# Performance work log

Hardware: AMD Instinct MI355X
Metric: run time of the kernel (lower is better)

The kernel has to match this reference:

```python
import jax, jax.numpy as jnp
import numpy as np

B, L, D, V, M = 8, 64, 256, 4096, 16


def _norm(a):
    # torch .std(-1) uses ddof=1 (unbiased)
    return a / (1e-5 + jnp.std(a, axis=-1, keepdims=True, ddof=1))


def setup_inputs() -> dict:
    key = jax.random.key(0)
    ks = jax.random.split(key, 13)
    s = 0.05
    return {
        "x": jax.random.randint(ks[0], (B, L), 0, V),
        "z": jax.random.randint(ks[1], (B, L), 0, V),
        "embed_w": jax.random.normal(ks[2], (V, D), dtype=jnp.float32) * s,
        "init_w": jax.random.normal(ks[3], (D, M), dtype=jnp.float32) * s,
        "trans_w": jax.random.normal(ks[4], (D, D), dtype=jnp.float32) * s,
        "trans_b": jax.random.normal(ks[5], (D,), dtype=jnp.float32) * s,
        "core_w": jax.random.normal(ks[6], (D, D), dtype=jnp.float32) * s,
        "upd_w": jax.random.normal(ks[7], (D, D), dtype=jnp.float32) * s,
        "xks_w": jax.random.normal(ks[8], (2, D), dtype=jnp.float32) * s,
        "xkd_w": jax.random.normal(ks[9], (D, D), dtype=jnp.float32) * s,
        "xkd_b": jax.random.normal(ks[10], (D,), dtype=jnp.float32) * s,
        "emi_w": jax.random.normal(ks[11], (D, D), dtype=jnp.float32) * s,
        "emi_b": jax.random.normal(ks[12], (D,), dtype=jnp.float32) * s,
    }


def reference(x, z, embed_w, init_w, trans_w, trans_b, core_w, upd_w,
              xks_w, xkd_w, xkd_b, emi_w, emi_b):
    # loss() sets y = x * 0 (all-zero token ids)
    ze = _norm(embed_w[z])                      # (B, L, D)
    ye = _norm(embed_w[x * 0])                  # (B, L, D)
    Bq, Lq, Dq = ze.shape

    # init_state.weight.T[None, 0:1] -> column 0, broadcast to (B, L, D), then norm
    xsa0 = _norm(jnp.broadcast_to(init_w[:, 0][None, None, :], (Bq, Lq, Dq)))

    def step(xsa, _):
        xnew = (jnp.roll(xsa, 1, axis=1) @ trans_w
                + jnp.roll(xsa, -1, axis=1) @ trans_w.T
                + xsa @ core_w
                + ze @ upd_w.T
                + trans_b) / 3.0
        return xnew, None

    xsa, _ = jax.lax.scan(step, xsa0, None, length=Lq)

    # mixture head
    xkey_static = jnp.broadcast_to(xks_w[None], (Bq, 2, Dq))          # (B, 2, D)
    xkey_dynamic = ye @ xkd_w.T + xkd_b                                # (B, L, D)
    xkey = jnp.concatenate([xkey_static, xkey_dynamic], axis=1)       # (B, 2+L, D)

    emit = xsa @ emi_w.T + emi_b                                       # (B, L, D)
    cand = jnp.concatenate(
        [emit[:, :, None], ze[:, :, None],
         jnp.broadcast_to(ye[:, None], (Bq, Lq, Lq, Dq))], axis=2)     # (B, L, 2+L, D)

    sel = jax.nn.log_softmax(jnp.einsum('bld,bkd->blk', xsa, xkey), axis=-1)  # (B, L, 2+L)
    lptok_c = jax.nn.log_softmax(cand @ embed_w.T, axis=-1)            # (B, L, 2+L, V)
    lptok = jax.nn.logsumexp(sel[..., None] + lptok_c, axis=-2)        # (B, L, V)
    lptok = jnp.exp(lptok / 2.0)

    cent = jnp.take_along_axis(lptok, x[:, :, None], axis=-1)[..., 0]  # (B, L)
    return -cent.mean(-1)                                              # (B,)
```

## Files before the change

kernel.cpp:

```cpp
#include <hip/hip_runtime.h>
#include <hip/hip_bf16.h>
#include <math.h>

#define BB 8
#define LL 64
#define DD 256
#define VV 4096
#define RR 512
#define K3 768

typedef __attribute__((ext_vector_type(4))) float f32x4;
typedef __attribute__((ext_vector_type(8))) short bf16x8;
typedef __attribute__((ext_vector_type(4))) unsigned short u16x4;
typedef unsigned long long u64;

#define WS_ZE      0
#define WS_ZEU3    (WS_ZE + RR*DD)
#define WS_WCT     (WS_ZEU3 + RR*DD)
#define WS_XSA0    (WS_WCT + DD*K3)
#define WS_XSA1    (WS_XSA0 + RR*DD)
#define WS_EMIT    (WS_XSA1 + RR*DD)
#define WS_YVEC    (WS_EMIT + RR*DD)
#define WS_X0VEC   (WS_YVEC + DD)
#define WS_YK      (WS_X0VEC + DD)
#define WS_YLOG    (WS_YK + DD)
#define WS_YLSE    (WS_YLOG + VV)
#define WS_SEL     (WS_YLSE + 8)
#define WS_TOKS    WS_SEL
#define WS_TWT     WS_XSA0
#define WS_CWT     (WS_XSA0 + 65536)
#define WS_EHI     861184
#define WS_ELO     (WS_EHI + VV*DD/2)
#define WS_HPHI    (WS_ELO + VV*DD/2)
#define WS_BIG_FLOATS (WS_HPHI + 1024*64*2)

__device__ __forceinline__ float waveSum(float v) {
#pragma unroll
  for (int o = 32; o > 0; o >>= 1) v += __shfl_xor(v, o, 64);
  return v;
}

__device__ __forceinline__ unsigned short f2bf(float f) {
  unsigned int u = __float_as_uint(f);
  unsigned int r = (u + 0x7fffu + ((u >> 16) & 1u)) >> 16;
  return (unsigned short)r;
}
__device__ __forceinline__ float bf2f(unsigned short h) {
  return __uint_as_float(((unsigned int)h) << 16);
}

union U64F2 { u64 u; float f[2]; };

__device__ __forceinline__ void head_tile(
    int row0, int vy, const float* __restrict__ uemit,
    const float* __restrict__ uze,
    const unsigned short* __restrict__ eh, const unsigned short* __restrict__ el,
    float* __restrict__ hpart, float* shbuf, int t) {
  unsigned short* UH = (unsigned short*)shbuf;
  unsigned short* UL = UH + 32 * 264;
  int lane = t & 63, w = t >> 6;
  int wr = w >> 1, wc = w & 1;
  const float* src = (row0 < RR) ? (uemit + (size_t)row0 * DD)
                                 : (uze + (size_t)(row0 - RR) * DD);
#pragma unroll
  for (int it = 0; it < 4; ++it) {
    int r = it * 8 + (t >> 5);
    int c8 = (t & 31) * 8;
    float4 a = *(const float4*)(src + (size_t)r * DD + c8);
    float4 b2 = *(const float4*)(src + (size_t)r * DD + c8 + 4);
    float fa[8] = {a.x, a.y, a.z, a.w, b2.x, b2.y, b2.z, b2.w};
    u16x4 h0, l0v, h1, l1;
#pragma unroll
    for (int j = 0; j < 4; ++j) {
      unsigned short hb = f2bf(fa[j]);
      h0[j] = hb; l0v[j] = f2bf(fa[j] - bf2f(hb));
      unsigned short hb1 = f2bf(fa[4 + j]);
      h1[j] = hb1; l1[j] = f2bf(fa[4 + j] - bf2f(hb1));
    }
    *(u16x4*)(&UH[r * 264 + c8])     = h0;
    *(u16x4*)(&UH[r * 264 + c8 + 4]) = h1;
    *(u16x4*)(&UL[r * 264 + c8])     = l0v;
    *(u16x4*)(&UL[r * 264 + c8 + 4]) = l1;
  }
  __syncthreads();

  f32x4 acc[4];
#pragma unroll
  for (int q = 0; q < 4; ++q) acc[q] = (f32x4){0.f, 0.f, 0.f, 0.f};

  int arow = wr * 16 + (lane & 15);
  int kof = 8 * (lane >> 4);
  const unsigned short* Ah = &UH[arow * 264 + kof];
  const unsigned short* Al = &UL[arow * 264 + kof];
  int vbase = vy * 128 + wc * 64 + (lane & 15);

#pragma unroll
  for (int p = 0; p < 3; ++p) {
    const unsigned short* Ab = (p == 2) ? Al : Ah;
    const unsigned short* Ebl = ((p == 1) ? el : eh) + (size_t)vbase * DD + kof;
#pragma unroll
    for (int ks = 0; ks < 8; ++ks) {
      int k0 = ks * 32;
      bf16x8 a = *(const bf16x8*)(Ab + k0);
#pragma unroll
      for (int vt = 0; vt < 4; ++vt) {
        bf16x8 bfr = *(const bf16x8*)(Ebl + vt * 16 * DD + k0);
        acc[vt] = __builtin_amdgcn_mfma_f32_16x16x32_bf16(a, bfr, acc[vt], 0, 0, 0);
      }
    }
  }

  int chunk = vy * 2 + wc;
#pragma unroll
  for (int i = 0; i < 4; ++i) {
    float mm = -1e30f;
#pragma unroll
    for (int vt = 0; vt < 4; ++vt) mm = fmaxf(mm, acc[vt][i]);
#pragma unroll
    for (int o = 1; o < 16; o <<= 1) mm = fmaxf(mm, __shfl_xor(mm, o, 64));
    float ss = 0.f;
#pragma unroll
    for (int vt = 0; vt < 4; ++vt) ss += __expf(acc[vt][i] - mm);
#pragma unroll
    for (int o = 1; o < 16; o <<= 1) ss += __shfl_xor(ss, o, 64);
    if ((lane & 15) == 0) {
      int row = row0 + wr * 16 + (lane >> 4) * 4 + i;
      hpart[((size_t)row * 64 + chunk) * 2]     = mm;
      hpart[((size_t)row * 64 + chunk) * 2 + 1] = ss;
    }
  }
}

__global__ __launch_bounds__(256) void k_prep1(
    const int* __restrict__ z, const float* __restrict__ embed,
    const float* __restrict__ initw, const float* __restrict__ tw,
    const float* __restrict__ cw, float* __restrict__ ws) {
  int bid = blockIdx.x, d = threadIdx.x;
  __shared__ float red[4];
  __shared__ float y[DD];
  if (bid < RR + 2) {
    float a; float* dst;
    if (bid < RR) { int tok = z[bid]; a = embed[tok * DD + d]; dst = ws + WS_ZE + bid * DD; }
    else if (bid == RR) { a = embed[d]; dst = ws + WS_YVEC; }
    else { a = initw[d * 16]; dst = ws + WS_X0VEC; }
    int lane = d & 63, w = d >> 6;
    float s = waveSum(a);
    __syncthreads();
    if (lane == 0) red[w] = s;
    __syncthreads();
    float sum = red[0] + red[1] + red[2] + red[3];
    float sq = waveSum(a * a);
    __syncthreads();
    if (lane == 0) red[w] = sq;
    __syncthreads();
    float sqs = red[0] + red[1] + red[2] + red[3];
    float mean = sum * (1.0f / DD);
    float var = fmaxf((sqs - (float)DD * mean * mean) * (1.0f / (DD - 1)), 0.0f);
    dst[d] = a / (1e-5f + sqrtf(var));
  } else if (bid < RR + 2 + 256) {
    int c = bid - (RR + 2);
    ws[WS_TWT + c * DD + d] = tw[d * DD + c];
    ws[WS_CWT + c * DD + d] = cw[d * DD + c];
  } else if (bid < RR + 2 + 256 + 1024) {
    int eb = bid - (RR + 2 + 256);
    unsigned short* eh = (unsigned short*)(ws + WS_EHI);
    unsigned short* el = (unsigned short*)(ws + WS_ELO);
    int i = (eb * 256 + d) * 4;
    float4 v = *(const float4*)(embed + i);
    float f[4] = {v.x, v.y, v.z, v.w};
    u16x4 h, l;
#pragma unroll
    for (int j = 0; j < 4; ++j) {
      unsigned short hb = f2bf(f[j]);
      h[j] = hb;
      l[j] = f2bf(f[j] - bf2f(hb));
    }
    *(u16x4*)(eh + i) = h;
    *(u16x4*)(el + i) = l;
  } else {
    int yb = bid - (RR + 2 + 256 + 1024);
    y[d] = ws[WS_YVEC + d];
    __syncthreads();
    int w = d >> 6, lane = d & 63;
    for (int i = 0; i < 16; i++) {
      int v = yb * 64 + i * 4 + w;
      float p = 0.f;
#pragma unroll
      for (int j = 0; j < 4; j++)
        p += y[lane + 64*j] * embed[(size_t)v * DD + lane + 64*j];
      p = waveSum(p);
      if (lane == 0) ws[WS_YLOG + v] = p;
    }
  }
}

__global__ __launch_bounds__(256) void k_prep0(
    const float* __restrict__ embed, const float* __restrict__ initw,
    float* __restrict__ ws) {
  int r = blockIdx.x, d = threadIdx.x;
  __shared__ float red[4];
  float a = (r == 0) ? embed[d] : initw[d * 16];
  float* dst = ws + ((r == 0) ? WS_YVEC : WS_X0VEC);
  int lane = d & 63, w = d >> 6;
  float s = waveSum(a);
  __syncthreads();
  if (lane == 0) red[w] = s;
  __syncthreads();
  float sum = red[0] + red[1] + red[2] + red[3];
  float sq = waveSum(a * a);
  __syncthreads();
  if (lane == 0) red[w] = sq;
  __syncthreads();
  float sqs = red[0] + red[1] + red[2] + red[3];
  float mean = sum * (1.0f / DD);
  float var = fmaxf((sqs - (float)DD * mean * mean) * (1.0f / (DD - 1)), 0.0f);
  dst[d] = a / (1e-5f + sqrtf(var));
}

__global__ __launch_bounds__(256) void k_rowmat2(
    const float* __restrict__ in, const float* __restrict__ W,
    const float* __restrict__ bias, float* __restrict__ out, float scale) {
  int r0 = blockIdx.x * 2, d = threadIdx.x;
  __shared__ float u[2][260];
  u[0][d] = in[r0 * DD + d];
  u[1][d] = in[(r0 + 1) * DD + d];
  __syncthreads();
  float a0 = 0.f, a1 = 0.f;
  const float4* w4 = (const float4*)(W + d * DD);
  const float4* u0 = (const float4*)&u[0][0];
  const float4* u1 = (const float4*)&u[1][0];
#pragma unroll 8
  for (int k4 = 0; k4 < 64; k4++) {
    float4 w = w4[k4], x0 = u0[k4], x1 = u1[k4];
    a0 += x0.x*w.x + x0.y*w.y + x0.z*w.z + x0.w*w.w;
    a1 += x1.x*w.x + x1.y*w.y + x1.z*w.z + x1.w*w.w;
  }
  float b = bias[d];
  out[r0 * DD + d]       = (a0 + b) * scale;
  out[(r0 + 1) * DD + d] = (a1 + b) * scale;
}

__global__ __launch_bounds__(256) void k_prep3(
    const float* __restrict__ tw, const float* __restrict__ cw,
    float* __restrict__ ws) {
  int bid = blockIdx.x, c = threadIdx.x;
  __shared__ float zs[4][260];
  __shared__ float rA[DD], rB[DD], rC[DD];
  if (bid < 256) {
    int r0 = bid * 2;
    int b = r0 >> 6, l = r0 & 63;
    const float* zb = ws + WS_ZEU3 + (size_t)b * 64 * DD;
    float* zout = ws + WS_XSA1;
#pragma unroll
    for (int j = 0; j < 4; ++j) {
      int ll = (l + j - 1 + 64) & 63;
      zs[j][c] = zb[ll * DD + c];
    }
    __syncthreads();
    const float4* wA = (const float4*)(ws + WS_TWT + (size_t)c * DD);
    const float4* wB = (const float4*)(tw + (size_t)c * DD);
    const float4* wC = (const float4*)(ws + WS_CWT + (size_t)c * DD);
    const float4* zm0 = (const float4*)&zs[0][0];
    const float4* z00 = (const float4*)&zs[1][0];
    const float4* zp0 = (const float4*)&zs[2][0];
    const float4* zp1 = (const float4*)&zs[3][0];
    float a0 = 0.f, a1 = 0.f;
#pragma unroll 8
    for (int k4 = 0; k4 < 64; ++k4) {
      float4 A4 = wA[k4], B4 = wB[k4], C4 = wC[k4];
      float4 m0 = zm0[k4], z0 = z00[k4], p0 = zp0[k4], p1 = zp1[k4];
      a0 += m0.x*A4.x + m0.y*A4.y + m0.z*A4.z + m0.w*A4.w
          + p0.x*B4.x + p0.y*B4.y + p0.z*B4.z + p0.w*B4.w
          + z0.x*C4.x + z0.y*C4.y + z0.z*C4.z + z0.w*C4.w;
      a1 += z0.x*A4.x + z0.y*A4.y + z0.z*A4.z + z0.w*A4.w
          + p1.x*B4.x + p1.y*B4.y + p1.z*B4.z + p1.w*B4.w
          + p0.x*C4.x + p0.y*C4.y + p0.z*C4.z + p0.w*C4.w;
    }
    const float inv3 = 1.0f / 3.0f;
    zout[(size_t)r0 * DD + c]       = a0 * inv3 + zs[1][c];
    zout[(size_t)(r0 + 1) * DD + c] = a1 * inv3 + zs[2][c];
  } else if (bid < 512) {
    int k = bid - 256;
    const float* twT = ws + WS_TWT;
    const float inv9 = 1.0f / 9.0f;
    rA[c] = tw[k * DD + c] * inv9;
    rB[c] = twT[k * DD + c] * inv9;
    rC[c] = cw[k * DD + c] * inv9;
    __syncthreads();
    float a2 = 0.f, m1 = 0.f, m0 = 0.f, m3 = 0.f, b2 = 0.f;
#pragma unroll 4
    for (int j = 0; j < DD; ++j) {
      float Aj = tw[j * DD + c];
      float Bj = twT[j * DD + c];
      float Cj = cw[j * DD + c];
      float ra = rA[j], rb = rB[j], rc = rC[j];
      a2 += ra * Aj;
      m1 += rc * Aj + ra * Cj;
      m0 += rb * Aj + ra * Bj + rc * Cj;
      m3 += rc * Bj + rb * Cj;
      b2 += rb * Bj;
    }
    float* p0 = ws + WS_WCT;
    float* p3 = ws + WS_ZEU3;
    p0[k * DD + c]               = a2;
    p0[65536 + k * DD + c]       = m1;
    p0[2 * 65536 + k * DD + c]   = m0;
    p3[k * DD + c]               = m3;
    p3[65536 + k * DD + c]       = b2;
  } else {
    ((int*)(ws + WS_TOKS))[(bid - 512) * 256 + c] = 0;
  }
}

__global__ __launch_bounds__(256, 2) void k_scan_big(
    float* __restrict__ ws, const float* __restrict__ emiw,
    const float* __restrict__ emib, const unsigned short* __restrict__ eh,
    const unsigned short* __restrict__ el, float* __restrict__ hpart) {
  const int bid = blockIdx.x;
  const int t = threadIdx.x, lane = t & 63;

  __shared__ float SH[12800];

  if (bid >= 512) {
    int eb = bid - 512;
    int row0 = RR + (eb & 15) * 32;
    int vy = eb >> 4;
    head_tile(row0, vy, ws + WS_EMIT, ws + WS_ZE, eh, el, hpart, SH, t);
    return;
  }

  float* S    = SH;
  float* PAR  = SH + 3168;
  float* PAR2 = SH + 11488;
  float* ZB   = SH + 12512;

  const int rg = bid & 63, cg = bid >> 6;
  const int b = rg >> 3, rgl = rg & 7, l0 = rgl * 8;
  const int cl = t & 7, rs = t >> 3;
  const int c0 = cg * 32 + cl * 4;

  int* tok = (int*)(ws + WS_TOKS);

  const float* Wp[5] = {ws + WS_WCT, ws + WS_WCT + 65536, ws + WS_WCT + 2*65536,
                        ws + WS_ZEU3, ws + WS_ZEU3 + 65536};
  f32x4 wreg[40];
#pragma unroll
  for (int p = 0; p < 5; ++p)
#pragma unroll
    for (int q = 0; q < 2; ++q)
#pragma unroll
      for (int kk = 0; kk < 4; ++kk)
        wreg[p * 8 + q * 4 + kk] =
            *(const f32x4*)&Wp[p][(size_t)(rs * 8 + q * 4 + kk) * DD + c0];

  {
    int r = t >> 5, c = t & 31;
    ZB[r * 32 + c] = ws[WS_XSA1 + (size_t)(b * 64 + l0 + r) * DD + cg * 32 + c];
  }

  const int nb0 = b * 8 + ((rgl + 7) & 7);
  const int nb1 = b * 8 + rgl;
  const int nb2 = b * 8 + ((rgl + 1) & 7);
  const int myl = (lane == 0) ? nb0 : (lane == 1) ? nb1 : nb2;

  for (int st = 0; st < 32; ++st) {
    const float* xin  = ws + ((st & 1) ? WS_XSA1 : WS_XSA0);
    float*       xout = ws + ((st & 1) ? WS_XSA0 : WS_XSA1);

    if (st > 0) {
      const int tg = st << 3;
      while (true) {
        int v = __hip_atomic_load(tok + myl * 32, __ATOMIC_RELAXED,
                                  __HIP_MEMORY_SCOPE_AGENT);
        if (__all(v >= tg)) break;
        __builtin_amdgcn_s_sleep(1);
      }
    }

#pragma unroll
    for (int it = 0; it < 6; ++it) {
      int idx = it * 256 + t;
      int j = idx >> 7;
      int kk = (idx & 127) << 1;
      const u64* src = (st == 0)
          ? (const u64*)(ws + WS_X0VEC + kk)
          : (const u64*)(xin + (size_t)(b * 64 + ((l0 + j - 2 + 64) & 63)) * DD + kk);
      u64 v = __hip_atomic_load(src, __ATOMIC_RELAXED, __HIP_MEMORY_SCOPE_AGENT);
      *(u64*)(&S[j * 264 + kk]) = v;
    }
    __syncthreads();

    f32x4 acc[8];
#pragma unroll
    for (int r = 0; r < 8; ++r) acc[r] = (f32x4){0.f, 0.f, 0.f, 0.f};

#pragma unroll
    for (int p = 0; p < 5; ++p) {
#pragma unroll
      for (int r = 0; r < 8; ++r) {
        int j = r + p;
#pragma unroll
        for (int q = 0; q < 2; ++q) {
          f32x4 xv = *(const f32x4*)&S[j * 264 + rs * 8 + q * 4];
          acc[r] += xv.x * wreg[p * 8 + q * 4 + 0];
          acc[r] += xv.y * wreg[p * 8 + q * 4 + 1];
          acc[r] += xv.z * wreg[p * 8 + q * 4 + 2];
          acc[r] += xv.w * wreg[p * 8 + q * 4 + 3];
        }
      }
    }

#pragma unroll
    for (int r = 0; r < 8; ++r)
      *(f32x4*)&PAR[rs * 260 + r * 32 + cl * 4] = acc[r];
    __syncthreads();

    {
      int u = t & 63, v = t >> 6;
      f32x4 s4 = (f32x4){0.f, 0.f, 0.f, 0.f};
#pragma unroll
      for (int i = 0; i < 8; ++i)
        s4 += *(const f32x4*)&PAR[(v * 8 + i) * 260 + u * 4];
      *(f32x4*)&PAR2[v * 256 + u * 4] = s4;
    }
    __syncthreads();

    if (t < 64) {
      int r = t >> 3, c8 = t & 7;
      f32x4 s4 = (f32x4){0.f, 0.f, 0.f, 0.f};
#pragma unroll
      for (int v = 0; v < 4; ++v)
        s4 += *(const f32x4*)&PAR2[v * 256 + t * 4];
      f32x4 zb = *(const f32x4*)&ZB[r * 32 + c8 * 4];
      s4 += zb;
      size_t off = (size_t)(b * 64 + l0 + r) * DD + cg * 32 + c8 * 4;
      U64F2 lo, hi;
      lo.f[0] = s4.x; lo.f[1] = s4.y;
      hi.f[0] = s4.z; hi.f[1] = s4.w;
      __hip_atomic_store((u64*)(xout + off),     lo.u, __ATOMIC_RELAXED, __HIP_MEMORY_SCOPE_AGENT);
      __hip_atomic_store((u64*)(xout + off + 2), hi.u, __ATOMIC_RELAXED, __HIP_MEMORY_SCOPE_AGENT);
    }

    __syncthreads();
    if (t == 0)
      __hip_atomic_fetch_add(tok + nb1 * 32, 1, __ATOMIC_RELAXED,
                             __HIP_MEMORY_SCOPE_AGENT);
  }

  if (t == 0) {
    while (__hip_atomic_load(tok + nb1 * 32, __ATOMIC_RELAXED,
                             __HIP_MEMORY_SCOPE_AGENT) < 256)
      __builtin_amdgcn_s_sleep(1);
  }
  __syncthreads();
#pragma unroll
  for (int it = 0; it < 4; ++it) {
    int idx = it * 256 + t;
    int j = idx >> 7;
    int kk = (idx & 127) << 1;
    u64 v = __hip_atomic_load(
        (const u64*)(ws + WS_XSA0 + (size_t)(b * 64 + l0 + j) * DD + kk),
        __ATOMIC_RELAXED, __HIP_MEMORY_SCOPE_AGENT);
    *(u64*)(&S[j * 264 + kk]) = v;
  }
  __syncthreads();
  {
    int r = t >> 5, c = cg * 32 + (t & 31);
    const float4* wv = (const float4*)(emiw + (size_t)c * DD);
    const float4* xv = (const float4*)&S[r * 264];
    float a = 0.f;
#pragma unroll 8
    for (int k4 = 0; k4 < 64; ++k4) {
      float4 w = wv[k4], x = xv[k4];
      a += x.x*w.x + x.y*w.y + x.z*w.z + x.w*w.w;
    }
    ws[WS_EMIT + (size_t)(b * 64 + l0 + r) * DD + c] = a + emib[c];
  }
}

__global__ __launch_bounds__(256) void k_head_mfma(
    const float* __restrict__ uemit, const float* __restrict__ uze,
    const unsigned short* __restrict__ eh, const unsigned short* __restrict__ el,
    float* __restrict__ hpart) {
  __shared__ float SH[8448];
  head_tile(blockIdx.x * 32, blockIdx.y, uemit, uze, eh, el, hpart, SH,
            threadIdx.x);
}

__global__ __launch_bounds__(256) void k_finish(
    const int* __restrict__ x, const float* __restrict__ embed,
    const float* __restrict__ xks, const float* __restrict__ xkdw,
    const float* __restrict__ xkdb, float* __restrict__ ws,
    const float* __restrict__ hp, float* __restrict__ out) {
  int b = blockIdx.x, t = threadIdx.x, lane = t & 63, w = t >> 6;
  __shared__ float YK[DD];
  __shared__ float rm[4], rv[4];
  __shared__ float ylse_s;
  __shared__ float sel0[64], sel1[64], sel2[64], tg0[64], tg1[64];
  __shared__ float ls0s[64], ls1s[64];

  {
    float acc = xkdb[t];
    const float4* yv4 = (const float4*)(ws + WS_YVEC);
    const float4* w4 = (const float4*)(xkdw + (size_t)t * DD);
    float a = 0.f;
#pragma unroll 8
    for (int k4 = 0; k4 < 64; ++k4) {
      float4 yv = yv4[k4], wv = w4[k4];
      a += yv.x*wv.x + yv.y*wv.y + yv.z*wv.z + yv.w*wv.w;
    }
    YK[t] = acc + a;
  }
  {
    float m = -1e30f, s = 0.f;
    for (int v = t; v < VV; v += 256) {
      float lg = ws[WS_YLOG + v];
      float mn = fmaxf(m, lg);
      s = s * __expf(m - mn) + __expf(lg - mn);
      m = mn;
    }
#pragma unroll
    for (int o = 32; o > 0; o >>= 1) {
      float mo = __shfl_xor(m, o, 64), so = __shfl_xor(s, o, 64);
      float mn = fmaxf(m, mo);
      s = s * __expf(m - mn) + so * __expf(mo - mn);
      m = mn;
    }
    if (lane == 0) { rm[w] = m; rv[w] = s; }
  }
  __syncthreads();
  if (t == 0) {
    float M = fmaxf(fmaxf(rm[0], rm[1]), fmaxf(rm[2], rm[3]));
    float S = rv[0]*__expf(rm[0]-M) + rv[1]*__expf(rm[1]-M) +
              rv[2]*__expf(rm[2]-M) + rv[3]*__expf(rm[3]-M);
    ylse_s = M + logf(S);
  }

  for (int i = 0; i < 16; ++i) {
    int l = w * 16 + i, r = b * 64 + l;
    float4 xs = *(const float4*)&ws[WS_XSA0 + (size_t)r * DD + lane * 4];
    float4 k0 = *(const float4*)&xks[lane * 4];
    float4 k1 = *(const float4*)&xks[DD + lane * 4];
    float4 yk4 = *(const float4*)&YK[lane * 4];
    float s0 = waveSum(xs.x*k0.x + xs.y*k0.y + xs.z*k0.z + xs.w*k0.w);
    float s1 = waveSum(xs.x*k1.x + xs.y*k1.y + xs.z*k1.z + xs.w*k1.w);
    float s2 = waveSum(xs.x*yk4.x + xs.y*yk4.y + xs.z*yk4.z + xs.w*yk4.w);
    int xv = x[r];
    float4 e4 = *(const float4*)&embed[(size_t)xv * DD + lane * 4];
    float4 em = *(const float4*)&ws[WS_EMIT + (size_t)r * DD + lane * 4];
    float4 zr = *(const float4*)&ws[WS_ZE + (size_t)r * DD + lane * 4];
    float t0 = waveSum(em.x*e4.x + em.y*e4.y + em.z*e4.z + em.w*e4.w);
    float t1 = waveSum(zr.x*e4.x + zr.y*e4.y + zr.z*e4.z + zr.w*e4.w);
    float m0 = hp[((size_t)r * 64 + lane) * 2];
    float q0 = hp[((size_t)r * 64 + lane) * 2 + 1];
    float m1 = hp[((size_t)(RR + r) * 64 + lane) * 2];
    float q1 = hp[((size_t)(RR + r) * 64 + lane) * 2 + 1];
#pragma unroll
    for (int o = 32; o > 0; o >>= 1) {
      float mo = __shfl_xor(m0, o, 64), so = __shfl_xor(q0, o, 64);
      float mn = fmaxf(m0, mo);
      q0 = q0 * __expf(m0 - mn) + so * __expf(mo - mn);
      m0 = mn;
      mo = __shfl_xor(m1, o, 64); so = __shfl_xor(q1, o, 64);
      mn = fmaxf(m1, mo);
      q1 = q1 * __expf(m1 - mn) + so * __expf(mo - mn);
      m1 = mn;
    }
    if (lane == 0) {
      sel0[l] = s0; sel1[l] = s1; sel2[l] = s2;
      tg0[l] = t0; tg1[l] = t1;
      ls0s[l] = m0 + logf(q0);
      ls1s[l] = m1 + logf(q1);
    }
  }
  __syncthreads();
  if (w == 0) {
    int l = lane, r = b * 64 + l;
    float s0 = sel0[l], s1 = sel1[l], s2 = sel2[l];
    float mx = fmaxf(s0, fmaxf(s1, s2));
    float den = expf(s0 - mx) + expf(s1 - mx) + 64.f * expf(s2 - mx);
    float lsel = mx + logf(den);
    int xv = x[r];
    float P0 = expf(s0 - lsel + tg0[l] - ls0s[l]);
    float P1 = expf(s1 - lsel + tg1[l] - ls1s[l]);
    float Py = expf(s2 - lsel + ws[WS_YLOG + xv] - ylse_s);
    float cent = sqrtf(P0 + P1 + 64.f * Py);
    float sum = waveSum(cent);
    if (lane == 0) out[b] = -(sum * (1.0f / 64.f));
  }
}

extern "C" void kernel_launch(void* const* d_in, const int* in_sizes, int n_in,
                              void* d_out, int out_size, void* d_ws, size_t ws_size,
                              hipStream_t stream) {
  (void)in_sizes; (void)n_in; (void)out_size;
  const int*   x     = (const int*)d_in[0];
  const int*   z     = (const int*)d_in[1];
  const float* embed = (const float*)d_in[2];
  const float* initw = (const float*)d_in[3];
  const float* tw    = (const float*)d_in[4];
  const float* tb    = (const float*)d_in[5];
  const float* cw    = (const float*)d_in[6];
  const float* uw    = (const float*)d_in[7];
  const float* xks   = (const float*)d_in[8];
  const float* xkdw  = (const float*)d_in[9];
  const float* xkdb  = (const float*)d_in[10];
  const float* emiw  = (const float*)d_in[11];
  const float* emib  = (const float*)d_in[12];
  float* ws  = (float*)d_ws;
  float* out = (float*)d_out;

  const bool big = ws_size >= (size_t)WS_BIG_FLOATS * sizeof(float);
  float* hpart = ws + (big ? WS_HPHI : WS_WCT);
  const unsigned short* ehg = (const unsigned short*)(ws + WS_EHI);
  const unsigned short* elg = (const unsigned short*)(ws + WS_ELO);

  hipLaunchKernelGGL(k_prep0, dim3(2), dim3(256), 0, stream, embed, initw, ws);
  hipLaunchKernelGGL(k_prep1, dim3(RR + 2 + 256 + 1024 + 64), dim3(256), 0,
                     stream, z, embed, initw, tw, cw, ws);
  hipLaunchKernelGGL(k_rowmat2, dim3(256), dim3(256), 0, stream,
                     ws + WS_ZE, uw, tb, ws + WS_ZEU3, 1.0f / 3.0f);
  hipLaunchKernelGGL(k_prep3, dim3(520), dim3(256), 0, stream, tw, cw, ws);
  hipLaunchKernelGGL(k_scan_big, dim3(big ? 1024 : 512), dim3(256), 0, stream,
                     ws, emiw, emib, ehg, elg, hpart);
  hipLaunchKernelGGL(k_head_mfma, dim3(big ? 16 : 32, 32), dim3(256), 0, stream,
                     ws + WS_EMIT, ws + WS_ZE, ehg, elg, hpart);
  hipLaunchKernelGGL(k_finish, dim3(8), dim3(256), 0, stream,
                     x, embed, xks, xkdw, xkdb, ws, hpart, out);
}
```

Baseline: 352.0 us.

## Replace shared atomic counter with per-block flag polling and drop fused head blocks

The scan kernel no longer runs extra head-tile blocks alongside the recurrence. The whole head GEMM now runs in the separate k_head_mfma launch over all 1024 rows. Cross-block synchronisation changes from one contended atomic fetch_add counter per row group to a separate step flag per producer block: each block stores st+1, and consumers poll 24 flags in parallel across lanes. This is meant to cut atomic contention and the spin latency per scan step, but it gives up the overlap of head work with the latency-bound scan.

Measured after the change: 360.6 us. 1.02x slower.

```diff
diff --git a/kernel.cpp b/kernel.cpp
--- a/kernel.cpp
+++ b/kernel.cpp
@@ -27,12 +27,11 @@
 #define WS_YLSE    (WS_YLOG + VV)
 #define WS_SEL     (WS_YLSE + 8)
 #define WS_TOKS    WS_SEL
+#define WS_HPART   WS_WCT
 #define WS_TWT     WS_XSA0
 #define WS_CWT     (WS_XSA0 + 65536)
 #define WS_EHI     861184
 #define WS_ELO     (WS_EHI + VV*DD/2)
-#define WS_HPHI    (WS_ELO + VV*DD/2)
-#define WS_BIG_FLOATS (WS_HPHI + 1024*64*2)
 
 __device__ __forceinline__ float waveSum(float v) {
 #pragma unroll
@@ -51,84 +50,27 @@
 
 union U64F2 { u64 u; float f[2]; };
 
-__device__ __forceinline__ void head_tile(
-    int row0, int vy, const float* __restrict__ uemit,
-    const float* __restrict__ uze,
-    const unsigned short* __restrict__ eh, const unsigned short* __restrict__ el,
-    float* __restrict__ hpart, float* shbuf, int t) {
-  unsigned short* UH = (unsigned short*)shbuf;
-  unsigned short* UL = UH + 32 * 264;
-  int lane = t & 63, w = t >> 6;
-  int wr = w >> 1, wc = w & 1;
-  const float* src = (row0 < RR) ? (uemit + (size_t)row0 * DD)
-                                 : (uze + (size_t)(row0 - RR) * DD);
-#pragma unroll
-  for (int it = 0; it < 4; ++it) {
-    int r = it * 8 + (t >> 5);
-    int c8 = (t & 31) * 8;
-    float4 a = *(const float4*)(src + (size_t)r * DD + c8);
-    float4 b2 = *(const float4*)(src + (size_t)r * DD + c8 + 4);
-    float fa[8] = {a.x, a.y, a.z, a.w, b2.x, b2.y, b2.z, b2.w};
-    u16x4 h0, l0v, h1, l1;
-#pragma unroll
-    for (int j = 0; j < 4; ++j) {
-      unsigned short hb = f2bf(fa[j]);
-      h0[j] = hb; l0v[j] = f2bf(fa[j] - bf2f(hb));
-      unsigned short hb1 = f2bf(fa[4 + j]);
-      h1[j] = hb1; l1[j] = f2bf(fa[4 + j] - bf2f(hb1));
-    }
-    *(u16x4*)(&UH[r * 264 + c8])     = h0;
-    *(u16x4*)(&UH[r * 264 + c8 + 4]) = h1;
-    *(u16x4*)(&UL[r * 264 + c8])     = l0v;
-    *(u16x4*)(&UL[r * 264 + c8 + 4]) = l1;
-  }
-  __syncthreads();
-
-  f32x4 acc[4];
-#pragma unroll
-  for (int q = 0; q < 4; ++q) acc[q] = (f32x4){0.f, 0.f, 0.f, 0.f};
-
-  int arow = wr * 16 + (lane & 15);
-  int kof = 8 * (lane >> 4);
-  const unsigned short* Ah = &UH[arow * 264 + kof];
-  const unsigned short* Al = &UL[arow * 264 + kof];
-  int vbase = vy * 128 + wc * 64 + (lane & 15);
-
-#pragma unroll
-  for (int p = 0; p < 3; ++p) {
-    const unsigned short* Ab = (p == 2) ? Al : Ah;
-    const unsigned short* Ebl = ((p == 1) ? el : eh) + (size_t)vbase * DD + kof;
-#pragma unroll
-    for (int ks = 0; ks < 8; ++ks) {
-      int k0 = ks * 32;
-      bf16x8 a = *(const bf16x8*)(Ab + k0);
-#pragma unroll
-      for (int vt = 0; vt < 4; ++vt) {
-        bf16x8 bfr = *(const bf16x8*)(Ebl + vt * 16 * DD + k0);
-        acc[vt] = __builtin_amdgcn_mfma_f32_16x16x32_bf16(a, bfr, acc[vt], 0, 0, 0);
-      }
-    }
-  }
-
-  int chunk = vy * 2 + wc;
-#pragma unroll
-  for (int i = 0; i < 4; ++i) {
-    float mm = -1e30f;
-#pragma unroll
-    for (int vt = 0; vt < 4; ++vt) mm = fmaxf(mm, acc[vt][i]);
-#pragma unroll
-    for (int o = 1; o < 16; o <<= 1) mm = fmaxf(mm, __shfl_xor(mm, o, 64));
-    float ss = 0.f;
-#pragma unroll
-    for (int vt = 0; vt < 4; ++vt) ss += __expf(acc[vt][i] - mm);
-#pragma unroll
-    for (int o = 1; o < 16; o <<= 1) ss += __shfl_xor(ss, o, 64);
-    if ((lane & 15) == 0) {
-      int row = row0 + wr * 16 + (lane >> 4) * 4 + i;
-      hpart[((size_t)row * 64 + chunk) * 2]     = mm;
-      hpart[((size_t)row * 64 + chunk) * 2 + 1] = ss;
-    }
-  }
+__global__ __launch_bounds__(256) void k_prep0(
+    const float* __restrict__ embed, const float* __restrict__ initw,
+    float* __restrict__ ws) {
+  int r = blockIdx.x, d = threadIdx.x;
+  __shared__ float red[4];
+  float a = (r == 0) ? embed[d] : initw[d * 16];
+  float* dst = ws + ((r == 0) ? WS_YVEC : WS_X0VEC);
+  int lane = d & 63, w = d >> 6;
+  float s = waveSum(a);
+  __syncthreads();
+  if (lane == 0) red[w] = s;
+  __syncthreads();
+  float sum = red[0] + red[1] + red[2] + red[3];
+  float sq = waveSum(a * a);
+  __syncthreads();
+  if (lane == 0) red[w] = sq;
+  __syncthreads();
+  float sqs = red[0] + red[1] + red[2] + red[3];
+  float mean = sum * (1.0f / DD);
+  float var = fmaxf((sqs - (float)DD * mean * mean) * (1.0f / (DD - 1)), 0.0f);
+  dst[d] = a / (1e-5f + sqrtf(var));
 }
 
 __global__ __launch_bounds__(256) void k_prep1(
@@ -192,29 +134,6 @@
       if (lane == 0) ws[WS_YLOG + v] = p;
     }
   }
-}
-
-__global__ __launch_bounds__(256) void k_prep0(
-    const float* __restrict__ embed, const float* __restrict__ initw,
-    float* __restrict__ ws) {
-  int r = blockIdx.x, d = threadIdx.x;
-  __shared__ float red[4];
-  float a = (r == 0) ? embed[d] : initw[d * 16];
-  float* dst = ws + ((r == 0) ? WS_YVEC : WS_X0VEC);
-  int lane = d & 63, w = d >> 6;
-  float s = waveSum(a);
-  __syncthreads();
-  if (lane == 0) red[w] = s;
-  __syncthreads();
-  float sum = red[0] + red[1] + red[2] + red[3];
-  float sq = waveSum(a * a);
-  __syncthreads();
-  if (lane == 0) red[w] = sq;
-  __syncthreads();
-  float sqs = red[0] + red[1] + red[2] + red[3];
-  float mean = sum * (1.0f / DD);
-  float var = fmaxf((sqs - (float)DD * mean * mean) * (1.0f / (DD - 1)), 0.0f);
-  dst[d] = a / (1e-5f + sqrtf(var));
 }
 
 __global__ __launch_bounds__(256) void k_rowmat2(
@@ -312,34 +231,29 @@
   }
 }
 
-__global__ __launch_bounds__(256, 2) void k_scan_big(
+__global__ __launch_bounds__(256, 2) void k_scan(
     float* __restrict__ ws, const float* __restrict__ emiw,
-    const float* __restrict__ emib, const unsigned short* __restrict__ eh,
-    const unsigned short* __restrict__ el, float* __restrict__ hpart) {
+    const float* __restrict__ emib) {
   const int bid = blockIdx.x;
-  const int t = threadIdx.x, lane = t & 63;
-
-  __shared__ float SH[12800];
-
-  if (bid >= 512) {
-    int eb = bid - 512;
-    int row0 = RR + (eb & 15) * 32;
-    int vy = eb >> 4;
-    head_tile(row0, vy, ws + WS_EMIT, ws + WS_ZE, eh, el, hpart, SH, t);
-    return;
-  }
-
-  float* S    = SH;
-  float* PAR  = SH + 3168;
-  float* PAR2 = SH + 11488;
-  float* ZB   = SH + 12512;
-
   const int rg = bid & 63, cg = bid >> 6;
   const int b = rg >> 3, rgl = rg & 7, l0 = rgl * 8;
+  const int t = threadIdx.x, lane = t & 63;
   const int cl = t & 7, rs = t >> 3;
   const int c0 = cg * 32 + cl * 4;
 
+  __shared__ float S[12 * 264];
+  __shared__ float PAR[32 * 260];
+  __shared__ float PAR2[4 * 256];
+  __shared__ float ZB[256];
+
   int* tok = (int*)(ws + WS_TOKS);
+  const int nb0 = b * 8 + ((rgl + 7) & 7);
+  const int nb1 = b * 8 + rgl;
+  const int nb2 = b * 8 + ((rgl + 1) & 7);
+  int pl = lane; if (pl >= 24) pl -= 24; if (pl >= 24) pl -= 24;
+  const int prg = (pl < 8) ? nb0 : (pl < 16) ? nb1 : nb2;
+  const int* pollAddr = tok + (prg * 8 + (pl & 7)) * 8;
+  int* myTok = tok + (nb1 * 8 + cg) * 8;
 
   const float* Wp[5] = {ws + WS_WCT, ws + WS_WCT + 65536, ws + WS_WCT + 2*65536,
                         ws + WS_ZEU3, ws + WS_ZEU3 + 65536};
@@ -358,21 +272,15 @@
     ZB[r * 32 + c] = ws[WS_XSA1 + (size_t)(b * 64 + l0 + r) * DD + cg * 32 + c];
   }
 
-  const int nb0 = b * 8 + ((rgl + 7) & 7);
-  const int nb1 = b * 8 + rgl;
-  const int nb2 = b * 8 + ((rgl + 1) & 7);
-  const int myl = (lane == 0) ? nb0 : (lane == 1) ? nb1 : nb2;
-
   for (int st = 0; st < 32; ++st) {
     const float* xin  = ws + ((st & 1) ? WS_XSA1 : WS_XSA0);
     float*       xout = ws + ((st & 1) ? WS_XSA0 : WS_XSA1);
 
     if (st > 0) {
-      const int tg = st << 3;
       while (true) {
-        int v = __hip_atomic_load(tok + myl * 32, __ATOMIC_RELAXED,
+        int v = __hip_atomic_load(pollAddr, __ATOMIC_RELAXED,
                                   __HIP_MEMORY_SCOPE_AGENT);
-        if (__all(v >= tg)) break;
+        if (__all(v >= st)) break;
         __builtin_amdgcn_s_sleep(1);
       }
     }
@@ -443,16 +351,18 @@
 
     __syncthreads();
     if (t == 0)
-      __hip_atomic_fetch_add(tok + nb1 * 32, 1, __ATOMIC_RELAXED,
-                             __HIP_MEMORY_SCOPE_AGENT);
-  }
-
-  if (t == 0) {
-    while (__hip_atomic_load(tok + nb1 * 32, __ATOMIC_RELAXED,
-                             __HIP_MEMORY_SCOPE_AGENT) < 256)
+      __hip_atomic_store(myTok, st + 1, __ATOMIC_RELAXED,
+                         __HIP_MEMORY_SCOPE_AGENT);
+  }
+
+  {
+    const int* ta = tok + (nb1 * 8 + (lane & 7)) * 8;
+    while (true) {
+      int v = __hip_atomic_load(ta, __ATOMIC_RELAXED, __HIP_MEMORY_SCOPE_AGENT);
+      if (__all(v >= 32)) break;
       __builtin_amdgcn_s_sleep(1);
-  }
-  __syncthreads();
+    }
+  }
 #pragma unroll
   for (int it = 0; it < 4; ++it) {
     int idx = it * 256 + t;
@@ -482,9 +392,81 @@
     const float* __restrict__ uemit, const float* __restrict__ uze,
     const unsigned short* __restrict__ eh, const unsigned short* __restrict__ el,
     float* __restrict__ hpart) {
-  __shared__ float SH[8448];
-  head_tile(blockIdx.x * 32, blockIdx.y, uemit, uze, eh, el, hpart, SH,
-            threadIdx.x);
+  int row0 = blockIdx.x * 32;
+  int v0 = blockIdx.y * 128;
+  int t = threadIdx.x, lane = t & 63, w = t >> 6;
+  int wr = w >> 1, wc = w & 1;
+  __shared__ unsigned short UH[32 * 264];
+  __shared__ unsigned short UL[32 * 264];
+  const float* src = (row0 < RR) ? (uemit + (size_t)row0 * DD)
+                                 : (uze + (size_t)(row0 - RR) * DD);
+#pragma unroll
+  for (int it = 0; it < 4; ++it) {
+    int r = it * 8 + (t >> 5);
+    int c8 = (t & 31) * 8;
+    float4 a = *(const float4*)(src + (size_t)r * DD + c8);
+    float4 b2 = *(const float4*)(src + (size_t)r * DD + c8 + 4);
+    float fa[8] = {a.x, a.y, a.z, a.w, b2.x, b2.y, b2.z, b2.w};
+    u16x4 h0, l0v, h1, l1;
+#pragma unroll
+    for (int j = 0; j < 4; ++j) {
+      unsigned short hb = f2bf(fa[j]);
+      h0[j] = hb; l0v[j] = f2bf(fa[j] - bf2f(hb));
+      unsigned short hb1 = f2bf(fa[4 + j]);
+      h1[j] = hb1; l1[j] = f2bf(fa[4 + j] - bf2f(hb1));
+    }
+    *(u16x4*)(&UH[r * 264 + c8])     = h0;
+    *(u16x4*)(&UH[r * 264 + c8 + 4]) = h1;
+    *(u16x4*)(&UL[r * 264 + c8])     = l0v;
+    *(u16x4*)(&UL[r * 264 + c8 + 4]) = l1;
+  }
+  __syncthreads();
+
+  f32x4 acc[4];
+#pragma unroll
+  for (int q = 0; q < 4; ++q) acc[q] = (f32x4){0.f, 0.f, 0.f, 0.f};
+
+  int arow = wr * 16 + (lane & 15);
+  int kof = 8 * (lane >> 4);
+  const unsigned short* Ah = &UH[arow * 264 + kof];
+  const unsigned short* Al = &UL[arow * 264 + kof];
+  int vbase = v0 + wc * 64 + (lane & 15);
+
+#pragma unroll
+  for (int p = 0; p < 3; ++p) {
+    const unsigned short* Ab = (p == 2) ? Al : Ah;
+    const unsigned short* Ebl = ((p == 1) ? el : eh) + (size_t)vbase * DD + kof;
+#pragma unroll
+    for (int ks = 0; ks < 8; ++ks) {
+      int k0 = ks * 32;
+      bf16x8 a = *(const bf16x8*)(Ab + k0);
+#pragma unroll
+      for (int vt = 0; vt < 4; ++vt) {
+        bf16x8 bfr = *(const bf16x8*)(Ebl + vt * 16 * DD + k0);
+        acc[vt] = __builtin_amdgcn_mfma_f32_16x16x32_bf16(a, bfr, acc[vt], 0, 0, 0);
+      }
+    }
+  }
+
+  int chunk = blockIdx.y * 2 + wc;
+#pragma unroll
+  for (int i = 0; i < 4; ++i) {
+    float mm = -1e30f;
+#pragma unroll
+    for (int vt = 0; vt < 4; ++vt) mm = fmaxf(mm, acc[vt][i]);
+#pragma unroll
+    for (int o = 1; o < 16; o <<= 1) mm = fmaxf(mm, __shfl_xor(mm, o, 64));
+    float ss = 0.f;
+#pragma unroll
+    for (int vt = 0; vt < 4; ++vt) ss += __expf(acc[vt][i] - mm);
+#pragma unroll
+    for (int o = 1; o < 16; o <<= 1) ss += __shfl_xor(ss, o, 64);
+    if ((lane & 15) == 0) {
+      int row = row0 + wr * 16 + (lane >> 4) * 4 + i;
+      hpart[((size_t)row * 64 + chunk) * 2]     = mm;
+      hpart[((size_t)row * 64 + chunk) * 2 + 1] = ss;
+    }
+  }
 }
 
 __global__ __launch_bounds__(256) void k_finish(
@@ -593,7 +575,7 @@
 extern "C" void kernel_launch(void* const* d_in, const int* in_sizes, int n_in,
                               void* d_out, int out_size, void* d_ws, size_t ws_size,
                               hipStream_t stream) {
-  (void)in_sizes; (void)n_in; (void)out_size;
+  (void)in_sizes; (void)n_in; (void)out_size; (void)ws_size;
   const int*   x     = (const int*)d_in[0];
   const int*   z     = (const int*)d_in[1];
   const float* embed = (const float*)d_in[2];
@@ -610,20 +592,18 @@
   float* ws  = (float*)d_ws;
   float* out = (float*)d_out;
 
-  const bool big = ws_size >= (size_t)WS_BIG_FLOATS * sizeof(float);
-  float* hpart = ws + (big ? WS_HPHI : WS_WCT);
   const unsigned short* ehg = (const unsigned short*)(ws + WS_EHI);
   const unsigned short* elg = (const unsigned short*)(ws + WS_ELO);
+  float* hpart = ws + WS_HPART;
 
   hipLaunchKernelGGL(k_prep0, dim3(2), dim3(256), 0, stream, embed, initw, ws);
   hipLaunchKernelGGL(k_prep1, dim3(RR + 2 + 256 + 1024 + 64), dim3(256), 0,
                      stream, z, embed, initw, tw, cw, ws);
   hipLaunchKernelGGL(k_rowmat2, dim3(256), dim3(256), 0, stream,
                      ws + WS_ZE, uw, tb, ws + WS_ZEU3, 1.0f / 3.0f);
-  hipLaunchKernelGGL(k_prep3, dim3(520), dim3(256), 0, stream, tw, cw, ws);
-  hipLaunchKernelGGL(k_scan_big, dim3(big ? 1024 : 512), dim3(256), 0, stream,
-                     ws, emiw, emib, ehg, elg, hpart);
-  hipLaunchKernelGGL(k_head_mfma, dim3(big ? 16 : 32, 32), dim3(256), 0, stream,
+  hipLaunchKernelGGL(k_prep3, dim3(528), dim3(256), 0, stream, tw, cw, ws);
+  hipLaunchKernelGGL(k_scan, dim3(512), dim3(256), 0, stream, ws, emiw, emib);
+  hipLaunchKernelGGL(k_head_mfma, dim3(32, 32), dim3(256), 0, stream,
                      ws + WS_EMIT, ws + WS_ZE, ehg, elg, hpart);
   hipLaunchKernelGGL(k_finish, dim3(8), dim3(256), 0, stream,
                      x, embed, xks, xkdw, xkdb, ws, hpart, out);
```

## Fuse head tiles into persistent scan kernel and merge prep launches

Applied to the files above, without the earlier changes.

Folds the ze·upd_w projection and the y-vector normalisation into k_prep1, which removes the k_prep0 and k_rowmat2 launches. The scan kernel now replaces its shared fetch-add counter with a per-column-group progress flag that waves poll in parallel. After the scan, each block computes a ze head tile and then an emit head tile once the neighbouring flags show the emit rows are ready, so the separate head launch is skipped when the workspace is large. This trades kernel-boundary overhead for spin-waiting inside a persistent grid, which depends on all 512 blocks being co-resident.

After: 355.1 us. About the same (+0.9%).

```diff
diff --git a/kernel.cpp b/kernel.cpp
--- a/kernel.cpp
+++ b/kernel.cpp
@@ -27,6 +27,7 @@
 #define WS_YLSE    (WS_YLOG + VV)
 #define WS_SEL     (WS_YLSE + 8)
 #define WS_TOKS    WS_SEL
+#define WS_HPART_SMALL WS_WCT
 #define WS_TWT     WS_XSA0
 #define WS_CWT     (WS_XSA0 + 65536)
 #define WS_EHI     861184
@@ -55,20 +56,33 @@
     int row0, int vy, const float* __restrict__ uemit,
     const float* __restrict__ uze,
     const unsigned short* __restrict__ eh, const unsigned short* __restrict__ el,
-    float* __restrict__ hpart, float* shbuf, int t) {
+    float* __restrict__ hpart, float* shbuf, int t, bool bypass) {
   unsigned short* UH = (unsigned short*)shbuf;
   unsigned short* UL = UH + 32 * 264;
   int lane = t & 63, w = t >> 6;
   int wr = w >> 1, wc = w & 1;
   const float* src = (row0 < RR) ? (uemit + (size_t)row0 * DD)
                                  : (uze + (size_t)(row0 - RR) * DD);
+  __syncthreads();
 #pragma unroll
   for (int it = 0; it < 4; ++it) {
     int r = it * 8 + (t >> 5);
     int c8 = (t & 31) * 8;
-    float4 a = *(const float4*)(src + (size_t)r * DD + c8);
-    float4 b2 = *(const float4*)(src + (size_t)r * DD + c8 + 4);
-    float fa[8] = {a.x, a.y, a.z, a.w, b2.x, b2.y, b2.z, b2.w};
+    float fa[8];
+    if (bypass) {
+#pragma unroll
+      for (int j = 0; j < 4; ++j) {
+        U64F2 v;
+        v.u = __hip_atomic_load((const u64*)(src + (size_t)r * DD + c8 + j * 2),
+                                __ATOMIC_RELAXED, __HIP_MEMORY_SCOPE_AGENT);
+        fa[j * 2] = v.f[0]; fa[j * 2 + 1] = v.f[1];
+      }
+    } else {
+      float4 a = *(const float4*)(src + (size_t)r * DD + c8);
+      float4 b2 = *(const float4*)(src + (size_t)r * DD + c8 + 4);
+      fa[0]=a.x; fa[1]=a.y; fa[2]=a.z; fa[3]=a.w;
+      fa[4]=b2.x; fa[5]=b2.y; fa[6]=b2.z; fa[7]=b2.w;
+    }
     u16x4 h0, l0v, h1, l1;
 #pragma unroll
     for (int j = 0; j < 4; ++j) {
@@ -134,10 +148,11 @@
 __global__ __launch_bounds__(256) void k_prep1(
     const int* __restrict__ z, const float* __restrict__ embed,
     const float* __restrict__ initw, const float* __restrict__ tw,
-    const float* __restrict__ cw, float* __restrict__ ws) {
+    const float* __restrict__ cw, const float* __restrict__ uw,
+    const float* __restrict__ tb, float* __restrict__ ws) {
   int bid = blockIdx.x, d = threadIdx.x;
   __shared__ float red[4];
-  __shared__ float y[DD];
+  __shared__ float u[260];
   if (bid < RR + 2) {
     float a; float* dst;
     if (bid < RR) { int tok = z[bid]; a = embed[tok * DD + d]; dst = ws + WS_ZE + bid * DD; }
@@ -156,7 +171,21 @@
     float sqs = red[0] + red[1] + red[2] + red[3];
     float mean = sum * (1.0f / DD);
     float var = fmaxf((sqs - (float)DD * mean * mean) * (1.0f / (DD - 1)), 0.0f);
-    dst[d] = a / (1e-5f + sqrtf(var));
+    float nv = a / (1e-5f + sqrtf(var));
+    dst[d] = nv;
+    if (bid < RR) {
+      u[d] = nv;
+      __syncthreads();
+      float a0 = 0.f;
+      const float4* w4 = (const float4*)(uw + (size_t)d * DD);
+      const float4* u0 = (const float4*)&u[0];
+#pragma unroll 8
+      for (int k4 = 0; k4 < 64; ++k4) {
+        float4 wv = w4[k4], x0 = u0[k4];
+        a0 += x0.x*wv.x + x0.y*wv.y + x0.z*wv.z + x0.w*wv.w;
+      }
+      ws[WS_ZEU3 + (size_t)bid * DD + d] = (a0 + tb[d]) * (1.0f / 3.0f);
+    }
   } else if (bid < RR + 2 + 256) {
     int c = bid - (RR + 2);
     ws[WS_TWT + c * DD + d] = tw[d * DD + c];
@@ -179,65 +208,32 @@
     *(u16x4*)(el + i) = l;
   } else {
     int yb = bid - (RR + 2 + 256 + 1024);
-    y[d] = ws[WS_YVEC + d];
-    __syncthreads();
-    int w = d >> 6, lane = d & 63;
+    float a = embed[d];
+    int lane = d & 63, w = d >> 6;
+    float s = waveSum(a);
+    __syncthreads();
+    if (lane == 0) red[w] = s;
+    __syncthreads();
+    float sum = red[0] + red[1] + red[2] + red[3];
+    float sq = waveSum(a * a);
+    __syncthreads();
+    if (lane == 0) red[w] = sq;
+    __syncthreads();
+    float sqs = red[0] + red[1] + red[2] + red[3];
+    float mean = sum * (1.0f / DD);
+    float var = fmaxf((sqs - (float)DD * mean * mean) * (1.0f / (DD - 1)), 0.0f);
+    u[d] = a / (1e-5f + sqrtf(var));
+    __syncthreads();
     for (int i = 0; i < 16; i++) {
       int v = yb * 64 + i * 4 + w;
       float p = 0.f;
 #pragma unroll
       for (int j = 0; j < 4; j++)
-        p += y[lane + 64*j] * embed[(size_t)v * DD + lane + 64*j];
+        p += u[lane + 64*j] * embed[(size_t)v * DD + lane + 64*j];
       p = waveSum(p);
       if (lane == 0) ws[WS_YLOG + v] = p;
     }
   }
-}
-
-__global__ __launch_bounds__(256) void k_prep0(
-    const float* __restrict__ embed, const float* __restrict__ initw,
-    float* __restrict__ ws) {
-  int r = blockIdx.x, d = threadIdx.x;
-  __shared__ float red[4];
-  float a = (r == 0) ? embed[d] : initw[d * 16];
-  float* dst = ws + ((r == 0) ? WS_YVEC : WS_X0VEC);
-  int lane = d & 63, w = d >> 6;
-  float s = waveSum(a);
-  __syncthreads();
-  if (lane == 0) red[w] = s;
-  __syncthreads();
-  float sum = red[0] + red[1] + red[2] + red[3];
-  float sq = waveSum(a * a);
-  __syncthreads();
-  if (lane == 0) red[w] = sq;
-  __syncthreads();
-  float sqs = red[0] + red[1] + red[2] + red[3];
-  float mean = sum * (1.0f / DD);
-  float var = fmaxf((sqs - (float)DD * mean * mean) * (1.0f / (DD - 1)), 0.0f);
-  dst[d] = a / (1e-5f + sqrtf(var));
-}
-
-__global__ __launch_bounds__(256) void k_rowmat2(
-    const float* __restrict__ in, const float* __restrict__ W,
-    const float* __restrict__ bias, float* __restrict__ out, float scale) {
-  int r0 = blockIdx.x * 2, d = threadIdx.x;
-  __shared__ float u[2][260];
-  u[0][d] = in[r0 * DD + d];
-  u[1][d] = in[(r0 + 1) * DD + d];
-  __syncthreads();
-  float a0 = 0.f, a1 = 0.f;
-  const float4* w4 = (const float4*)(W + d * DD);
-  const float4* u0 = (const float4*)&u[0][0];
-  const float4* u1 = (const float4*)&u[1][0];
-#pragma unroll 8
-  for (int k4 = 0; k4 < 64; k4++) {
-    float4 w = w4[k4], x0 = u0[k4], x1 = u1[k4];
-    a0 += x0.x*w.x + x0.y*w.y + x0.z*w.z + x0.w*w.w;
-    a1 += x1.x*w.x + x1.y*w.y + x1.z*w.z + x1.w*w.w;
-  }
-  float b = bias[d];
-  out[r0 * DD + d]       = (a0 + b) * scale;
-  out[(r0 + 1) * DD + d] = (a1 + b) * scale;
 }
 
 __global__ __launch_bounds__(256) void k_prep3(
@@ -312,34 +308,32 @@
   }
 }
 
-__global__ __launch_bounds__(256, 2) void k_scan_big(
+__global__ __launch_bounds__(256, 2) void k_scan(
     float* __restrict__ ws, const float* __restrict__ emiw,
     const float* __restrict__ emib, const unsigned short* __restrict__ eh,
-    const unsigned short* __restrict__ el, float* __restrict__ hpart) {
+    const unsigned short* __restrict__ el, float* __restrict__ hpart,
+    int doHead) {
   const int bid = blockIdx.x;
+  const int rg = bid & 63, cg = bid >> 6;
+  const int b = rg >> 3, rgl = rg & 7, l0 = rgl * 8;
   const int t = threadIdx.x, lane = t & 63;
+  const int cl = t & 7, rs = t >> 3;
+  const int c0 = cg * 32 + cl * 4;
 
   __shared__ float SH[12800];
-
-  if (bid >= 512) {
-    int eb = bid - 512;
-    int row0 = RR + (eb & 15) * 32;
-    int vy = eb >> 4;
-    head_tile(row0, vy, ws + WS_EMIT, ws + WS_ZE, eh, el, hpart, SH, t);
-    return;
-  }
-
   float* S    = SH;
   float* PAR  = SH + 3168;
   float* PAR2 = SH + 11488;
   float* ZB   = SH + 12512;
 
-  const int rg = bid & 63, cg = bid >> 6;
-  const int b = rg >> 3, rgl = rg & 7, l0 = rgl * 8;
-  const int cl = t & 7, rs = t >> 3;
-  const int c0 = cg * 32 + cl * 4;
-
   int* tok = (int*)(ws + WS_TOKS);
+  const int nb0 = b * 8 + ((rgl + 7) & 7);
+  const int nb1 = b * 8 + rgl;
+  const int nb2 = b * 8 + ((rgl + 1) & 7);
+  int pl = lane; if (pl >= 24) pl -= 24; if (pl >= 24) pl -= 24;
+  const int prg = (pl < 8) ? nb0 : (pl < 16) ? nb1 : nb2;
+  const int* pollAddr = tok + (prg * 8 + (pl & 7)) * 8;
+  int* myTok = tok + (nb1 * 8 + cg) * 8;
 
   const float* Wp[5] = {ws + WS_WCT, ws + WS_WCT + 65536, ws + WS_WCT + 2*65536,
                         ws + WS_ZEU3, ws + WS_ZEU3 + 65536};
@@ -358,21 +352,15 @@
     ZB[r * 32 + c] = ws[WS_XSA1 + (size_t)(b * 64 + l0 + r) * DD + cg * 32 + c];
   }
 
-  const int nb0 = b * 8 + ((rgl + 7) & 7);
-  const int nb1 = b * 8 + rgl;
-  const int nb2 = b * 8 + ((rgl + 1) & 7);
-  const int myl = (lane == 0) ? nb0 : (lane == 1) ? nb1 : nb2;
-
   for (int st = 0; st < 32; ++st) {
     const float* xin  = ws + ((st & 1) ? WS_XSA1 : WS_XSA0);
     float*       xout = ws + ((st & 1) ? WS_XSA0 : WS_XSA1);
 
     if (st > 0) {
-      const int tg = st << 3;
       while (true) {
-        int v = __hip_atomic_load(tok + myl * 32, __ATOMIC_RELAXED,
+        int v = __hip_atomic_load(pollAddr, __ATOMIC_RELAXED,
                                   __HIP_MEMORY_SCOPE_AGENT);
-        if (__all(v >= tg)) break;
+        if (__all(v >= st)) break;
         __builtin_amdgcn_s_sleep(1);
       }
     }
@@ -443,16 +431,18 @@
 
     __syncthreads();
     if (t == 0)
-      __hip_atomic_fetch_add(tok + nb1 * 32, 1, __ATOMIC_RELAXED,
-                             __HIP_MEMORY_SCOPE_AGENT);
-  }
-
-  if (t == 0) {
-    while (__hip_atomic_load(tok + nb1 * 32, __ATOMIC_RELAXED,
-                             __HIP_MEMORY_SCOPE_AGENT) < 256)
+      __hip_atomic_store(myTok, st + 1, __ATOMIC_RELAXED,
+                         __HIP_MEMORY_SCOPE_AGENT);
+  }
+
+  {
+    const int* ta = tok + (nb1 * 8 + (lane & 7)) * 8;
+    while (true) {
+      int v = __hip_atomic_load(ta, __ATOMIC_RELAXED, __HIP_MEMORY_SCOPE_AGENT);
+      if (__all(v >= 32)) break;
       __builtin_amdgcn_s_sleep(1);
-  }
-  __syncthreads();
+    }
+  }
 #pragma unroll
   for (int it = 0; it < 4; ++it) {
     int idx = it * 256 + t;
@@ -464,9 +454,10 @@
     *(u64*)(&S[j * 264 + kk]) = v;
   }
   __syncthreads();
+  float* EM = PAR;
   {
-    int r = t >> 5, c = cg * 32 + (t & 31);
-    const float4* wv = (const float4*)(emiw + (size_t)c * DD);
+    int r = t >> 5, c = t & 31;
+    const float4* wv = (const float4*)(emiw + (size_t)(cg * 32 + c) * DD);
     const float4* xv = (const float4*)&S[r * 264];
     float a = 0.f;
 #pragma unroll 8
@@ -474,7 +465,40 @@
       float4 w = wv[k4], x = xv[k4];
       a += x.x*w.x + x.y*w.y + x.z*w.z + x.w*w.w;
     }
-    ws[WS_EMIT + (size_t)(b * 64 + l0 + r) * DD + c] = a + emib[c];
+    EM[r * 32 + c] = a + emib[cg * 32 + c];
+  }
+  __syncthreads();
+  if (t < 128) {
+    int r = t >> 4, c2 = (t & 15) * 2;
+    U64F2 v;
+    v.f[0] = EM[r * 32 + c2];
+    v.f[1] = EM[r * 32 + c2 + 1];
+    __hip_atomic_store(
+        (u64*)(ws + WS_EMIT + (size_t)(b * 64 + l0 + r) * DD + cg * 32 + c2),
+        v.u, __ATOMIC_RELAXED, __HIP_MEMORY_SCOPE_AGENT);
+  }
+  __syncthreads();
+  if (t == 0)
+    __hip_atomic_store(myTok, 33, __ATOMIC_RELAXED, __HIP_MEMORY_SCOPE_AGENT);
+
+  if (!doHead) return;
+
+  {
+    int T1 = bid + 512;
+    head_tile((T1 >> 5) * 32, T1 & 31, ws + WS_EMIT, ws + WS_ZE,
+              eh, el, hpart, SH, t, false);
+  }
+  {
+    int ri0 = bid >> 5, vc0 = bid & 31;
+    int pl2 = lane & 31;
+    const int* ta = tok + ((ri0 * 4 + (pl2 >> 3)) * 8 + (pl2 & 7)) * 8;
+    while (true) {
+      int v = __hip_atomic_load(ta, __ATOMIC_RELAXED, __HIP_MEMORY_SCOPE_AGENT);
+      if (__all(v >= 33)) break;
+      __builtin_amdgcn_s_sleep(1);
+    }
+    head_tile(ri0 * 32, vc0, ws + WS_EMIT, ws + WS_ZE,
+              eh, el, hpart, SH, t, true);
   }
 }
 
@@ -484,7 +508,7 @@
     float* __restrict__ hpart) {
   __shared__ float SH[8448];
   head_tile(blockIdx.x * 32, blockIdx.y, uemit, uze, eh, el, hpart, SH,
-            threadIdx.x);
+            threadIdx.x, false);
 }
 
 __global__ __launch_bounds__(256) void k_finish(
@@ -611,20 +635,19 @@
   float* out = (float*)d_out;
 
   const bool big = ws_size >= (size_t)WS_BIG_FLOATS * sizeof(float);
-  float* hpart = ws + (big ? WS_HPHI : WS_WCT);
+  float* hpart = ws + (big ? WS_HPHI : WS_HPART_SMALL);
   const unsigned short* ehg = (const unsigned short*)(ws + WS_EHI);
   const unsigned short* elg = (const unsigned short*)(ws + WS_ELO);
 
-  hipLaunchKernelGGL(k_prep0, dim3(2), dim3(256), 0, stream, embed, initw, ws);
   hipLaunchKernelGGL(k_prep1, dim3(RR + 2 + 256 + 1024 + 64), dim3(256), 0,
-                     stream, z, embed, initw, tw, cw, ws);
-  hipLaunchKernelGGL(k_rowmat2, dim3(256), dim3(256), 0, stream,
-                     ws + WS_ZE, uw, tb, ws + WS_ZEU3, 1.0f / 3.0f);
-  hipLaunchKernelGGL(k_prep3, dim3(520), dim3(256), 0, stream, tw, cw, ws);
-  hipLaunchKernelGGL(k_scan_big, dim3(big ? 1024 : 512), dim3(256), 0, stream,
-                     ws, emiw, emib, ehg, elg, hpart);
-  hipLaunchKernelGGL(k_head_mfma, dim3(big ? 16 : 32, 32), dim3(256), 0, stream,
-                     ws + WS_EMIT, ws + WS_ZE, ehg, elg, hpart);
+                     stream, z, embed, initw, tw, cw, uw, tb, ws);
+  hipLaunchKernelGGL(k_prep3, dim3(528), dim3(256), 0, stream, tw, cw, ws);
+  hipLaunchKernelGGL(k_scan, dim3(512), dim3(256), 0, stream,
+                     ws, emiw, emib, ehg, elg, hpart, big ? 1 : 0);
+  if (!big) {
+    hipLaunchKernelGGL(k_head_mfma, dim3(32, 32), dim3(256), 0, stream,
+                       ws + WS_EMIT, ws + WS_ZE, ehg, elg, hpart);
+  }
   hipLaunchKernelGGL(k_finish, dim3(8), dim3(256), 0, stream,
                      x, embed, xks, xkdw, xkdb, ws, hpart, out);
 }
```
